# Optimization experiments

Hardware: AMD Instinct MI355X
Metric: run time of the kernel (lower is better)

Reference implementation:

```python
import jax, jax.numpy as jnp
import numpy as np

B, TQ, TKV, D, H = 4, 1024, 1024, 1024, 16
HD = D // H  # head_size = 64
EPS = 1e-5


def setup_inputs() -> dict:
    key = jax.random.key(0)
    ks = jax.random.split(key, 5)
    s = 0.02
    return {
        "x_q": jax.random.normal(ks[0], (B, TQ, D), jnp.float32),
        "x_kv": jax.random.normal(ks[1], (B, TKV, D), jnp.float32),
        "Wq": jax.random.normal(ks[2], (D, 2 * D), jnp.float32) * s,
        "Wkv": jax.random.normal(ks[3], (D, 3 * D), jnp.float32) * s,
        "Wc": jax.random.normal(ks[4], (D, D), jnp.float32) * s,
        "qn1": jnp.ones((HD,), jnp.float32),
        "kn1": jnp.ones((HD,), jnp.float32),
        "qn2": jnp.ones((HD,), jnp.float32),
        "kn2": jnp.ones((HD,), jnp.float32),
        "gn_w": jnp.ones((D,), jnp.float32),
        "gn_b": jnp.zeros((D,), jnp.float32),
        "lmb": jnp.full((1, H, 1, 1), -4.0, jnp.float32),
    }


def _rms(x, w):
    # RMSNorm over last dim (head_size), eps=1e-5, learned scale w
    return x * jax.lax.rsqrt(jnp.mean(x * x, axis=-1, keepdims=True) + EPS) * w


def _heads(t, T):
    # (B,T,D) -> (B,H,T,HD)
    return t.reshape(B, T, H, HD).transpose(0, 2, 1, 3)


def _attn(q, k, v):
    att = jnp.einsum('bhqd,bhkd->bhqk', q, k) * (1.0 / np.sqrt(HD))
    att = jax.nn.softmax(att, axis=-1)
    return jnp.einsum('bhqk,bhkd->bhqd', att, v)


def reference(x_q, x_kv, Wq, Wkv, Wc, qn1, kn1, qn2, kn2, gn_w, gn_b, lmb):
    q1, q2 = jnp.split(x_q @ Wq, 2, axis=-1)
    k1, k2, v = jnp.split(x_kv @ Wkv, 3, axis=-1)
    q1 = _rms(_heads(q1, TQ), qn1)
    q2 = _rms(_heads(q2, TQ), qn2)
    k1 = _rms(_heads(k1, TKV), kn1)
    k2 = _rms(_heads(k2, TKV), kn2)
    v = _heads(v, TKV)
    y = _attn(q1, k1, v) - jax.nn.softplus(lmb) * _attn(q2, k2, v)  # (B,H,TQ,HD)
    # GroupNorm(n_head groups over n_embd channels), input (B,C,TQ):
    # per (batch, head) stats over (TQ, HD)
    mu = jnp.mean(y, axis=(2, 3), keepdims=True)
    var = jnp.var(y, axis=(2, 3), keepdims=True)
    yn = (y - mu) * jax.lax.rsqrt(var + EPS)
    yn = yn * gn_w.reshape(1, H, 1, HD) + gn_b.reshape(1, H, 1, HD)
    y = yn.transpose(0, 2, 1, 3).reshape(B, TQ, D)
    return y @ Wc
```

## Files before the change

kernel.cpp:

```cpp
#include <hip/hip_runtime.h>
#include <cstdint>
#include <cstddef>

#define B_ 4
#define TQ_ 1024
#define TKV_ 1024
#define D_ 1024
#define H_ 16
#define HD_ 64

typedef __bf16 bf16_t;
typedef bf16_t bf16x4 __attribute__((ext_vector_type(4)));
typedef bf16_t bf16x8 __attribute__((ext_vector_type(8)));
typedef float f32x4 __attribute__((ext_vector_type(4)));

#if __has_builtin(__builtin_amdgcn_exp2f)
#define EXP2F __builtin_amdgcn_exp2f
#else
#define EXP2F exp2f
#endif

__device__ __forceinline__ bf16_t to_bf16(float f) {
  uint32_t u = __builtin_bit_cast(uint32_t, f);
  u += 0x7fffu + ((u >> 16) & 1u);
  uint16_t h = (uint16_t)(u >> 16);
  return __builtin_bit_cast(bf16_t, h);
}
__device__ __forceinline__ float bf2f(bf16_t b) {
  uint32_t u = ((uint32_t)__builtin_bit_cast(uint16_t, b)) << 16;
  return __builtin_bit_cast(float, u);
}
__device__ __forceinline__ uint32_t pack_bf16_trunc(float lo, float hi) {
  return __builtin_amdgcn_perm(__builtin_bit_cast(uint32_t, hi),
                               __builtin_bit_cast(uint32_t, lo), 0x07060302u);
}
__device__ __forceinline__ void gload_lds16(const void* g, void* l) {
  __builtin_amdgcn_global_load_lds((const __attribute__((address_space(1))) void*)g,
                                   (__attribute__((address_space(3))) void*)l, 16, 0, 0);
}

__global__ __launch_bounds__(256) void k_prep(const float* __restrict__ xq,
                                              const float* __restrict__ xkv,
                                              const float* __restrict__ Wq,
                                              const float* __restrict__ Wkv,
                                              const float* __restrict__ Wc,
                                              bf16_t* __restrict__ oq,
                                              bf16_t* __restrict__ okv,
                                              bf16_t* __restrict__ Wqt,
                                              bf16_t* __restrict__ Wkvt,
                                              bf16_t* __restrict__ Wct,
                                              float* __restrict__ part) {
  int blk = blockIdx.x;
  if (blk == 0 && threadIdx.x < 128) part[threadIdx.x] = 0.f;
  if (blk < 8192) {
    const float* in = (blk < 4096) ? xq : xkv;
    bf16_t* out = (blk < 4096) ? oq : okv;
    int i = (blk & 4095) * 256 + threadIdx.x;
    float4 v = ((const float4*)in)[i];
    bf16x4 o = {to_bf16(v.x), to_bf16(v.y), to_bf16(v.z), to_bf16(v.w)};
    *(bf16x4*)(out + (size_t)i * 4) = o;
  } else {
    __shared__ float tile[32][33];
    int t = blk - 8192;
    int x = t % 192, yb = t / 192;
    const float* in;
    bf16_t* out;
    int C, c0;
    if (x < 64) { in = Wq; out = Wqt; C = 2048; c0 = x * 32; }
    else if (x < 160) { in = Wkv; out = Wkvt; C = 3072; c0 = (x - 64) * 32; }
    else { in = Wc; out = Wct; C = 1024; c0 = (x - 160) * 32; }
    int r0 = yb * 32;
    int tx = threadIdx.x & 31, ty = threadIdx.x >> 5;
#pragma unroll
    for (int i = 0; i < 4; i++)
      tile[ty + i * 8][tx] = in[(size_t)(r0 + ty + i * 8) * C + c0 + tx];
    __syncthreads();
#pragma unroll
    for (int i = 0; i < 4; i++) {
      int rr = ty + i * 8;
      out[(size_t)(c0 + rr) * 1024 + r0 + tx] = to_bf16(tile[tx][rr]);
    }
  }
}

__global__ __launch_bounds__(256, 2) void k_gemm_qkv(const bf16_t* __restrict__ xq,
                                                     const bf16_t* __restrict__ xkv,
                                                     const bf16_t* __restrict__ Wqt,
                                                     const bf16_t* __restrict__ Wkvt,
                                                     const float* __restrict__ kn1,
                                                     const float* __restrict__ kn2,
                                                     bf16_t* __restrict__ q12,
                                                     bf16_t* __restrict__ k1h,
                                                     bf16_t* __restrict__ k2h,
                                                     bf16_t* __restrict__ vt) {
  __shared__ bf16_t As[128 * 32];
  __shared__ bf16_t Bs[128 * 32];
  const int tid = threadIdx.x;
  const int wave = tid >> 6, lane = tid & 63;
  const int ln = lane & 15, lq = lane >> 4;

  const int fid = blockIdx.x;
  const int xcd = fid & 7, l = fid >> 3;
  bool isq;
  int xb, yb;
  if (l < 64) {
    isq = true;
    xb = (xcd & 3) * 4 + (l & 3);
    yb = (xcd >> 2) * 16 + (l >> 2);
  } else {
    isq = false;
    int l2 = l - 64;
    xb = (xcd & 3) * 6 + l2 % 6;
    yb = (xcd >> 2) * 16 + l2 / 6;
  }
  const bf16_t* A = isq ? xq : xkv;
  const bf16_t* Bt = isq ? Wqt : Wkvt;
  const int n0 = xb * 128, m0 = yb * 128;
  const int wm = (wave >> 1) * 64, wn = (wave & 1) * 64;
  f32x4 acc[4][4];
#pragma unroll
  for (int i = 0; i < 4; i++)
#pragma unroll
    for (int j = 0; j < 4; j++) acc[i][j] = (f32x4){0.f, 0.f, 0.f, 0.f};

  for (int k0 = 0; k0 < 1024; k0 += 32) {
#pragma unroll
    for (int rnd = 0; rnd < 2; rnd++) {
      int c = rnd * 256 + tid;
      int row = c >> 2, col = (c & 3) * 8;
      int ldsoff = (rnd * 256 + wave * 64) * 16;
      gload_lds16(A + (size_t)(m0 + row) * 1024 + k0 + col, (char*)As + ldsoff);
      gload_lds16(Bt + (size_t)(n0 + row) * 1024 + k0 + col, (char*)Bs + ldsoff);
    }
    asm volatile("s_waitcnt vmcnt(0)" ::: "memory");
    __syncthreads();
    bf16x8 af[4], bfr[4];
#pragma unroll
    for (int i = 0; i < 4; i++) {
      af[i] = *(const bf16x8*)(As + (wm + i * 16 + ln) * 32 + lq * 8);
      bfr[i] = *(const bf16x8*)(Bs + (wn + i * 16 + ln) * 32 + lq * 8);
    }
#pragma unroll
    for (int i = 0; i < 4; i++)
#pragma unroll
      for (int j = 0; j < 4; j++)
        acc[i][j] = __builtin_amdgcn_mfma_f32_16x16x32_bf16(af[i], bfr[j], acc[i][j], 0, 0, 0);
    __syncthreads();
  }

  if (isq) {
#pragma unroll
    for (int i = 0; i < 4; i++)
#pragma unroll
      for (int j = 0; j < 4; j++)
#pragma unroll
        for (int r = 0; r < 4; r++) {
          int row = m0 + wm + i * 16 + lq * 4 + r;
          int col = n0 + wn + j * 16 + ln;
          q12[(size_t)row * 2048 + col] = to_bf16(acc[i][j][r]);
        }
  } else {
    const int col0 = n0 + wn;
    const int part3 = col0 >> 10;
    const int h = (col0 >> 6) & 15;
    const int b = m0 >> 10;
    const int bh = b * 16 + h;
    if (part3 < 2) {
      const float* kn = part3 ? kn2 : kn1;
      bf16_t* dst = part3 ? k2h : k1h;
      float kw[4];
#pragma unroll
      for (int j = 0; j < 4; j++) kw[j] = kn[j * 16 + ln];
#pragma unroll
      for (int i = 0; i < 4; i++)
#pragma unroll
        for (int r = 0; r < 4; r++) {
          float ss = 0.f;
#pragma unroll
          for (int j = 0; j < 4; j++) ss += acc[i][j][r] * acc[i][j][r];
          ss += __shfl_xor(ss, 1, 64);
          ss += __shfl_xor(ss, 2, 64);
          ss += __shfl_xor(ss, 4, 64);
          ss += __shfl_xor(ss, 8, 64);
          float rstd = rsqrtf(ss * (1.f / 64.f) + 1e-5f);
          int m = m0 + wm + i * 16 + lq * 4 + r;
          int t = m & 1023;
          size_t base = ((size_t)bh * 1024 + t) * 64;
#pragma unroll
          for (int j = 0; j < 4; j++)
            dst[base + j * 16 + ln] = to_bf16(acc[i][j][r] * rstd * kw[j]);
        }
    } else {
      bf16_t* obase = vt + (size_t)bh * 65536;
#pragma unroll
      for (int i = 0; i < 4; i++) {
        int t0 = (m0 & 1023) + wm + i * 16 + lq * 4;
        int tp = (t0 & ~31) | (((t0 >> 2) & 3) << 3) | (((t0 >> 4) & 1) << 2);
#pragma unroll
        for (int j = 0; j < 4; j++) {
          bf16x4 pv;
#pragma unroll
          for (int r = 0; r < 4; r++) pv[r] = to_bf16(acc[i][j][r]);
          *(bf16x4*)(obase + (size_t)(j * 16 + ln) * 1024 + tp) = pv;
        }
      }
    }
  }
}

__global__ __launch_bounds__(256, 2) void k_gemm64(const bf16_t* __restrict__ A,
                                                   const bf16_t* __restrict__ Bt,
                                                   float* __restrict__ C, int N, int K) {
  __shared__ bf16_t As[128 * 32];
  __shared__ bf16_t Bs[64 * 32];
  const int tid = threadIdx.x;
  const int wave = tid >> 6, lane = tid & 63;
  const int ln = lane & 15, lq = lane >> 4;
  const int fid = blockIdx.x;
  const int xcd = fid & 7, l = fid >> 3;
  const int lx = l & 1, ly = (l >> 1) & 15, yh = l >> 5;
  const int n0 = (xcd * 2 + lx) * 64;
  const int m0 = (yh * 16 + ly) * 128;
  const int wm = wave * 32;
  f32x4 acc[2][4];
#pragma unroll
  for (int i = 0; i < 2; i++)
#pragma unroll
    for (int j = 0; j < 4; j++) acc[i][j] = (f32x4){0.f, 0.f, 0.f, 0.f};

  for (int k0 = 0; k0 < K; k0 += 32) {
#pragma unroll
    for (int rnd = 0; rnd < 2; rnd++) {
      int c = rnd * 256 + tid;
      int row = c >> 2, col = (c & 3) * 8;
      int ldsoff = (rnd * 256 + wave * 64) * 16;
      gload_lds16(A + (size_t)(m0 + row) * K + k0 + col, (char*)As + ldsoff);
    }
    {
      int row = tid >> 2, col = (tid & 3) * 8;
      int ldsoff = (wave * 64) * 16;
      gload_lds16(Bt + (size_t)(n0 + row) * K + k0 + col, (char*)Bs + ldsoff);
    }
    asm volatile("s_waitcnt vmcnt(0)" ::: "memory");
    __syncthreads();
    bf16x8 af[2], bfr[4];
#pragma unroll
    for (int i = 0; i < 2; i++)
      af[i] = *(const bf16x8*)(As + (wm + i * 16 + ln) * 32 + lq * 8);
#pragma unroll
    for (int j = 0; j < 4; j++)
      bfr[j] = *(const bf16x8*)(Bs + (j * 16 + ln) * 32 + lq * 8);
#pragma unroll
    for (int i = 0; i < 2; i++)
#pragma unroll
      for (int j = 0; j < 4; j++)
        acc[i][j] = __builtin_amdgcn_mfma_f32_16x16x32_bf16(af[i], bfr[j], acc[i][j], 0, 0, 0);
    __syncthreads();
  }
#pragma unroll
  for (int i = 0; i < 2; i++)
#pragma unroll
    for (int j = 0; j < 4; j++)
#pragma unroll
      for (int r = 0; r < 4; r++) {
        int row = m0 + wm + i * 16 + lq * 4 + r;
        int col = n0 + j * 16 + ln;
        C[(size_t)row * N + col] = acc[i][j][r];
      }
}

__global__ __launch_bounds__(256, 2) void k_attn2(const bf16_t* __restrict__ q12,
                                                  const bf16_t* __restrict__ k1h,
                                                  const bf16_t* __restrict__ k2h,
                                                  const bf16_t* __restrict__ vt,
                                                  const float* __restrict__ qn1,
                                                  const float* __restrict__ qn2,
                                                  const float* __restrict__ lmb,
                                                  bf16_t* __restrict__ y,
                                                  float* __restrict__ part) {
  __shared__ bf16_t Ks[2][4096];
  __shared__ bf16_t Vs[4096];
  __shared__ float red[8];
  const int tid = threadIdx.x;
  const int wave = tid >> 6, lane = tid & 63;
  const int ln = lane & 15, lq = lane >> 4;
  const int swz = ln & 7;
  const int bh = blockIdx.x;
  const int b = bh >> 4, h = bh & 15;
  const int q0 = blockIdx.y * 128 + wave * 32;
  const bf16_t* kb[2] = {k1h + (size_t)bh * 65536, k2h + (size_t)bh * 65536};
  const bf16_t* vb = vt + (size_t)bh * 65536;

  bf16x8 qf[2][2][2];
#pragma unroll
  for (int st = 0; st < 2; st++)
#pragma unroll
    for (int mt = 0; mt < 2; mt++)
#pragma unroll
      for (int ks = 0; ks < 2; ks++)
        qf[st][mt][ks] = *(const bf16x8*)(q12 + (size_t)(b * 1024 + q0 + mt * 16 + ln) * 2048 +
                                          st * 1024 + h * 64 + ks * 32 + lq * 8);
#pragma unroll
  for (int st = 0; st < 2; st++)
#pragma unroll
    for (int mt = 0; mt < 2; mt++) {
      const float* qn = st ? qn2 : qn1;
      float ssq = 0.f;
#pragma unroll
      for (int ks = 0; ks < 2; ks++)
#pragma unroll
        for (int j = 0; j < 8; j++) {
          float v = bf2f(qf[st][mt][ks][j]);
          ssq += v * v;
        }
      ssq += __shfl_xor(ssq, 16, 64);
      ssq += __shfl_xor(ssq, 32, 64);
      float rr = rsqrtf(ssq * (1.f / 64.f) + 1e-5f) * (0.125f * 1.44269504f);
#pragma unroll
      for (int ks = 0; ks < 2; ks++)
#pragma unroll
        for (int j = 0; j < 8; j++)
          qf[st][mt][ks][j] = to_bf16(bf2f(qf[st][mt][ks][j]) * rr * qn[ks * 32 + lq * 8 + j]);
    }

  f32x4 O[2][2][4];
  float lp[2][2] = {{0.f, 0.f}, {0.f, 0.f}};
#pragma unroll
  for (int st = 0; st < 2; st++)
#pragma unroll
    for (int mt = 0; mt < 2; mt++)
#pragma unroll
      for (int nt = 0; nt < 4; nt++) O[st][mt][nt] = (f32x4){0.f, 0.f, 0.f, 0.f};

  for (int kv0 = 0; kv0 < TKV_; kv0 += 64) {
    __syncthreads();
#pragma unroll
    for (int r = 0; r < 6; r++) {
      int a = r >> 1, r2 = r & 1;
      int g = r2 * 256 + tid;
      int row = g >> 3;
      int blk = (g & 7) ^ (row & 7);
      const bf16_t* src = (a < 2) ? (kb[a] + (size_t)(kv0 + row) * 64 + blk * 8)
                                  : (vb + (size_t)row * 1024 + kv0 + blk * 8);
      char* dst = (a < 2) ? ((char*)Ks + a * 8192) : (char*)Vs;
      gload_lds16(src, dst + (r2 * 256 + wave * 64) * 16);
    }
    asm volatile("s_waitcnt vmcnt(0)" ::: "memory");
    __syncthreads();

    bf16x8 vf[2][4];
#pragma unroll
    for (int u = 0; u < 2; u++)
#pragma unroll
      for (int nt = 0; nt < 4; nt++)
        vf[u][nt] = *(const bf16x8*)(Vs + ((nt * 16 + ln) * 8 + ((u * 4 + lq) ^ swz)) * 8);

#pragma unroll
    for (int st = 0; st < 2; st++) {
      bf16x8 kf[2][4];
#pragma unroll
      for (int ks = 0; ks < 2; ks++)
#pragma unroll
        for (int t = 0; t < 4; t++)
          kf[ks][t] = *(const bf16x8*)(&Ks[st][((t * 16 + ln) * 8 + ((4 * ks + lq) ^ swz)) * 8]);
#pragma unroll
      for (int mt = 0; mt < 2; mt++) {
        f32x4 s[4];
#pragma unroll
        for (int t = 0; t < 4; t++) s[t] = (f32x4){0.f, 0.f, 0.f, 0.f};
#pragma unroll
        for (int ks = 0; ks < 2; ks++)
#pragma unroll
          for (int t = 0; t < 4; t++)
            s[t] = __builtin_amdgcn_mfma_f32_16x16x32_bf16(kf[ks][t], qf[st][mt][ks], s[t], 0, 0, 0);
        uint32_t pfu[2][4];
        float l = 0.f;
#pragma unroll
        for (int t = 0; t < 4; t++) {
          float e0 = EXP2F(s[t][0]), e1 = EXP2F(s[t][1]);
          float e2 = EXP2F(s[t][2]), e3 = EXP2F(s[t][3]);
          l += (e0 + e1) + (e2 + e3);
          pfu[t >> 1][(t & 1) * 2] = pack_bf16_trunc(e0, e1);
          pfu[t >> 1][(t & 1) * 2 + 1] = pack_bf16_trunc(e2, e3);
        }
        lp[st][mt] += l;
#pragma unroll
        for (int u = 0; u < 2; u++) {
          bf16x8 pf = __builtin_bit_cast(bf16x8, *(uint4*)pfu[u]);
#pragma unroll
          for (int nt = 0; nt < 4; nt++)
            O[st][mt][nt] =
                __builtin_amdgcn_mfma_f32_16x16x32_bf16(pf, vf[u][nt], O[st][mt][nt], 0, 0, 0);
        }
      }
    }
  }

  float c = log1pf(__expf(lmb[h]));
  float s_acc = 0.f, ss_acc = 0.f;
#pragma unroll
  for (int mt = 0; mt < 2; mt++) {
    float linv[2][4];
#pragma unroll
    for (int st = 0; st < 2; st++) {
      float l = lp[st][mt];
      l += __shfl_xor(l, 16, 64);
      l += __shfl_xor(l, 32, 64);
#pragma unroll
      for (int r = 0; r < 4; r++) linv[st][r] = 1.f / __shfl(l, lq * 4 + r, 64);
    }
#pragma unroll
    for (int nt = 0; nt < 4; nt++)
#pragma unroll
      for (int r = 0; r < 4; r++) {
        size_t a = ((size_t)bh * TQ_ + q0 + mt * 16 + lq * 4 + r) * 64 + nt * 16 + ln;
        float val = O[0][mt][nt][r] * linv[0][r] - c * O[1][mt][nt][r] * linv[1][r];
        s_acc += val;
        ss_acc += val * val;
        y[a] = to_bf16(val);
      }
  }
#pragma unroll
  for (int m = 1; m < 64; m <<= 1) {
    s_acc += __shfl_xor(s_acc, m, 64);
    ss_acc += __shfl_xor(ss_acc, m, 64);
  }
  if (lane == 0) {
    red[wave] = s_acc;
    red[4 + wave] = ss_acc;
  }
  __syncthreads();
  if (tid == 0) {
    atomicAdd(&part[bh * 2], red[0] + red[1] + red[2] + red[3]);
    atomicAdd(&part[bh * 2 + 1], red[4] + red[5] + red[6] + red[7]);
  }
}

__global__ __launch_bounds__(256) void k_gn_apply(const bf16_t* __restrict__ y,
                                                  const float* __restrict__ part,
                                                  const float* __restrict__ gw,
                                                  const float* __restrict__ gb,
                                                  bf16_t* __restrict__ yn) {
  int idx = blockIdx.x * 256 + threadIdx.x;
  int i = idx * 8;
  int bh = i >> 16;
  int h = bh & 15, b = bh >> 4;
  float S = part[bh * 2], SS = part[bh * 2 + 1];
  float mean = S * (1.f / 65536.f);
  float var = SS * (1.f / 65536.f) - mean * mean;
  float rstd = rsqrtf(var + 1e-5f);
  bf16x8 a = *(const bf16x8*)(y + i);
  int rem = i & 65535;
  int t = rem >> 6, d = rem & 63;
  bf16x8 o;
#pragma unroll
  for (int j = 0; j < 8; j++) {
    float f = (bf2f(a[j]) - mean) * rstd * gw[h * 64 + d + j] + gb[h * 64 + d + j];
    o[j] = to_bf16(f);
  }
  *(bf16x8*)(yn + ((size_t)(b * 1024 + t)) * 1024 + h * 64 + d) = o;
}

extern "C" void kernel_launch(void* const* d_in, const int* in_sizes, int n_in,
                              void* d_out, int out_size, void* d_ws, size_t ws_size,
                              hipStream_t stream) {
  const float* x_q = (const float*)d_in[0];
  const float* x_kv = (const float*)d_in[1];
  const float* Wq = (const float*)d_in[2];
  const float* Wkv = (const float*)d_in[3];
  const float* Wc = (const float*)d_in[4];
  const float* qn1 = (const float*)d_in[5];
  const float* kn1 = (const float*)d_in[6];
  const float* qn2 = (const float*)d_in[7];
  const float* kn2 = (const float*)d_in[8];
  const float* gn_w = (const float*)d_in[9];
  const float* gn_b = (const float*)d_in[10];
  const float* lmb = (const float*)d_in[11];

  const size_t MB = (size_t)1 << 20;
  char* ws = (char*)d_ws;
  bf16_t* xq_bf = (bf16_t*)(ws + 0 * MB);
  bf16_t* xkv_bf = (bf16_t*)(ws + 8 * MB);
  bf16_t* Wqt = (bf16_t*)(ws + 16 * MB);
  bf16_t* Wkvt = (bf16_t*)(ws + 20 * MB);
  bf16_t* Wct = (bf16_t*)(ws + 26 * MB);
  bf16_t* q12 = (bf16_t*)(ws + 28 * MB);
  bf16_t* k1h = (bf16_t*)(ws + 44 * MB);
  bf16_t* k2h = (bf16_t*)(ws + 52 * MB);
  bf16_t* vt = (bf16_t*)(ws + 60 * MB);
  bf16_t* y = (bf16_t*)(ws + 68 * MB);
  bf16_t* yn = (bf16_t*)(ws + 76 * MB);
  float* part = (float*)(ws + 84 * MB);

  k_prep<<<14336, 256, 0, stream>>>(x_q, x_kv, Wq, Wkv, Wc, xq_bf, xkv_bf, Wqt, Wkvt, Wct,
                                    part);
  k_gemm_qkv<<<1280, 256, 0, stream>>>(xq_bf, xkv_bf, Wqt, Wkvt, kn1, kn2, q12, k1h, k2h,
                                       vt);
  k_attn2<<<dim3(64, 8), 256, 0, stream>>>(q12, k1h, k2h, vt, qn1, qn2, lmb, y, part);
  k_gn_apply<<<2048, 256, 0, stream>>>(y, part, gn_w, gn_b, yn);
  k_gemm64<<<512, 256, 0, stream>>>(yn, Wct, (float*)d_out, 1024, 1024);
}
```

Before: 238.3 us.

## Double K-step depth in GEMMs and attention, add XOR-swizzled LDS layout

The QKV and output GEMMs now stage 64-wide K slices per iteration instead of 32. Their LDS tiles use an XOR swizzle on 16-byte chunks to avoid bank conflicts. The attention kernel loads 128 KV rows per iteration instead of 64 and processes them in two inner chunks. The aim is to halve the number of barrier/wait round trips and add LDS bank-conflict avoidance in the GEMMs. The cost is doubled shared memory per block, which could lower occupancy below the two blocks per CU the launch bounds target.

```diff
diff --git a/kernel.cpp b/kernel.cpp
--- a/kernel.cpp
+++ b/kernel.cpp
@@ -93,11 +93,12 @@
                                                      bf16_t* __restrict__ k1h,
                                                      bf16_t* __restrict__ k2h,
                                                      bf16_t* __restrict__ vt) {
-  __shared__ bf16_t As[128 * 32];
-  __shared__ bf16_t Bs[128 * 32];
+  __shared__ bf16_t As[128 * 64];
+  __shared__ bf16_t Bs[128 * 64];
   const int tid = threadIdx.x;
   const int wave = tid >> 6, lane = tid & 63;
   const int ln = lane & 15, lq = lane >> 4;
+  const int swz = ln & 7;
 
   const int fid = blockIdx.x;
   const int xcd = fid & 7, l = fid >> 3;
@@ -123,28 +124,33 @@
 #pragma unroll
     for (int j = 0; j < 4; j++) acc[i][j] = (f32x4){0.f, 0.f, 0.f, 0.f};
 
-  for (int k0 = 0; k0 < 1024; k0 += 32) {
-#pragma unroll
-    for (int rnd = 0; rnd < 2; rnd++) {
-      int c = rnd * 256 + tid;
-      int row = c >> 2, col = (c & 3) * 8;
-      int ldsoff = (rnd * 256 + wave * 64) * 16;
-      gload_lds16(A + (size_t)(m0 + row) * 1024 + k0 + col, (char*)As + ldsoff);
-      gload_lds16(Bt + (size_t)(n0 + row) * 1024 + k0 + col, (char*)Bs + ldsoff);
+  for (int k0 = 0; k0 < 1024; k0 += 64) {
+#pragma unroll
+    for (int r = 0; r < 8; r++) {
+      int g = (r & 3) * 256 + tid;
+      int row = g >> 3;
+      int dg = (g & 7) ^ (row & 7);
+      const bf16_t* src = (r < 4) ? (A + (size_t)(m0 + row) * 1024 + k0 + dg * 8)
+                                  : (Bt + (size_t)(n0 + row) * 1024 + k0 + dg * 8);
+      char* dst = ((r < 4) ? (char*)As : (char*)Bs) + ((r & 3) * 256 + wave * 64) * 16;
+      gload_lds16(src, dst);
     }
     asm volatile("s_waitcnt vmcnt(0)" ::: "memory");
     __syncthreads();
-    bf16x8 af[4], bfr[4];
-#pragma unroll
-    for (int i = 0; i < 4; i++) {
-      af[i] = *(const bf16x8*)(As + (wm + i * 16 + ln) * 32 + lq * 8);
-      bfr[i] = *(const bf16x8*)(Bs + (wn + i * 16 + ln) * 32 + lq * 8);
-    }
-#pragma unroll
-    for (int i = 0; i < 4; i++)
-#pragma unroll
-      for (int j = 0; j < 4; j++)
-        acc[i][j] = __builtin_amdgcn_mfma_f32_16x16x32_bf16(af[i], bfr[j], acc[i][j], 0, 0, 0);
+#pragma unroll
+    for (int ks = 0; ks < 2; ks++) {
+      bf16x8 af[4], bfr[4];
+#pragma unroll
+      for (int i = 0; i < 4; i++) {
+        af[i] = *(const bf16x8*)(As + ((wm + i * 16 + ln) * 8 + ((ks * 4 + lq) ^ swz)) * 8);
+        bfr[i] = *(const bf16x8*)(Bs + ((wn + i * 16 + ln) * 8 + ((ks * 4 + lq) ^ swz)) * 8);
+      }
+#pragma unroll
+      for (int i = 0; i < 4; i++)
+#pragma unroll
+        for (int j = 0; j < 4; j++)
+          acc[i][j] = __builtin_amdgcn_mfma_f32_16x16x32_bf16(af[i], bfr[j], acc[i][j], 0, 0, 0);
+    }
     __syncthreads();
   }
 
@@ -211,11 +217,12 @@
 __global__ __launch_bounds__(256, 2) void k_gemm64(const bf16_t* __restrict__ A,
                                                    const bf16_t* __restrict__ Bt,
                                                    float* __restrict__ C, int N, int K) {
-  __shared__ bf16_t As[128 * 32];
-  __shared__ bf16_t Bs[64 * 32];
+  __shared__ bf16_t As[128 * 64];
+  __shared__ bf16_t Bs[64 * 64];
   const int tid = threadIdx.x;
   const int wave = tid >> 6, lane = tid & 63;
   const int ln = lane & 15, lq = lane >> 4;
+  const int swz = ln & 7;
   const int fid = blockIdx.x;
   const int xcd = fid & 7, l = fid >> 3;
   const int lx = l & 1, ly = (l >> 1) & 15, yh = l >> 5;
@@ -228,33 +235,35 @@
 #pragma unroll
     for (int j = 0; j < 4; j++) acc[i][j] = (f32x4){0.f, 0.f, 0.f, 0.f};
 
-  for (int k0 = 0; k0 < K; k0 += 32) {
-#pragma unroll
-    for (int rnd = 0; rnd < 2; rnd++) {
-      int c = rnd * 256 + tid;
-      int row = c >> 2, col = (c & 3) * 8;
-      int ldsoff = (rnd * 256 + wave * 64) * 16;
-      gload_lds16(A + (size_t)(m0 + row) * K + k0 + col, (char*)As + ldsoff);
-    }
-    {
-      int row = tid >> 2, col = (tid & 3) * 8;
-      int ldsoff = (wave * 64) * 16;
-      gload_lds16(Bt + (size_t)(n0 + row) * K + k0 + col, (char*)Bs + ldsoff);
+  for (int k0 = 0; k0 < K; k0 += 64) {
+#pragma unroll
+    for (int r = 0; r < 6; r++) {
+      int g = ((r < 4) ? (r & 3) : (r - 4)) * 256 + tid;
+      int row = g >> 3;
+      int dg = (g & 7) ^ (row & 7);
+      const bf16_t* src = (r < 4) ? (A + (size_t)(m0 + row) * K + k0 + dg * 8)
+                                  : (Bt + (size_t)(n0 + row) * K + k0 + dg * 8);
+      char* dst = ((r < 4) ? (char*)As + (r & 3) * 4096 : (char*)Bs + (r - 4) * 4096) +
+                  (wave * 64) * 16;
+      gload_lds16(src, dst);
     }
     asm volatile("s_waitcnt vmcnt(0)" ::: "memory");
     __syncthreads();
-    bf16x8 af[2], bfr[4];
-#pragma unroll
-    for (int i = 0; i < 2; i++)
-      af[i] = *(const bf16x8*)(As + (wm + i * 16 + ln) * 32 + lq * 8);
-#pragma unroll
-    for (int j = 0; j < 4; j++)
-      bfr[j] = *(const bf16x8*)(Bs + (j * 16 + ln) * 32 + lq * 8);
-#pragma unroll
-    for (int i = 0; i < 2; i++)
+#pragma unroll
+    for (int ks = 0; ks < 2; ks++) {
+      bf16x8 af[2], bfr[4];
+#pragma unroll
+      for (int i = 0; i < 2; i++)
+        af[i] = *(const bf16x8*)(As + ((wm + i * 16 + ln) * 8 + ((ks * 4 + lq) ^ swz)) * 8);
 #pragma unroll
       for (int j = 0; j < 4; j++)
-        acc[i][j] = __builtin_amdgcn_mfma_f32_16x16x32_bf16(af[i], bfr[j], acc[i][j], 0, 0, 0);
+        bfr[j] = *(const bf16x8*)(Bs + ((j * 16 + ln) * 8 + ((ks * 4 + lq) ^ swz)) * 8);
+#pragma unroll
+      for (int i = 0; i < 2; i++)
+#pragma unroll
+        for (int j = 0; j < 4; j++)
+          acc[i][j] = __builtin_amdgcn_mfma_f32_16x16x32_bf16(af[i], bfr[j], acc[i][j], 0, 0, 0);
+    }
     __syncthreads();
   }
 #pragma unroll
@@ -278,8 +287,8 @@
                                                   const float* __restrict__ lmb,
                                                   bf16_t* __restrict__ y,
                                                   float* __restrict__ part) {
-  __shared__ bf16_t Ks[2][4096];
-  __shared__ bf16_t Vs[4096];
+  __shared__ bf16_t Ks[2][8192];
+  __shared__ bf16_t Vs[8192];
   __shared__ float red[8];
   const int tid = threadIdx.x;
   const int wave = tid >> 6, lane = tid & 63;
@@ -332,65 +341,78 @@
 #pragma unroll
       for (int nt = 0; nt < 4; nt++) O[st][mt][nt] = (f32x4){0.f, 0.f, 0.f, 0.f};
 
-  for (int kv0 = 0; kv0 < TKV_; kv0 += 64) {
-    __syncthreads();
-#pragma unroll
-    for (int r = 0; r < 6; r++) {
-      int a = r >> 1, r2 = r & 1;
-      int g = r2 * 256 + tid;
-      int row = g >> 3;
-      int blk = (g & 7) ^ (row & 7);
-      const bf16_t* src = (a < 2) ? (kb[a] + (size_t)(kv0 + row) * 64 + blk * 8)
-                                  : (vb + (size_t)row * 1024 + kv0 + blk * 8);
-      char* dst = (a < 2) ? ((char*)Ks + a * 8192) : (char*)Vs;
-      gload_lds16(src, dst + (r2 * 256 + wave * 64) * 16);
+  for (int kv0 = 0; kv0 < TKV_; kv0 += 128) {
+    __syncthreads();
+#pragma unroll
+    for (int r = 0; r < 12; r++) {
+      int reg = r >> 2;
+      int g = (r & 3) * 256 + tid;
+      const bf16_t* src;
+      if (reg < 2) {
+        int row = g >> 3;
+        int dg = (g & 7) ^ (row & 7);
+        src = kb[reg] + (size_t)(kv0 + row) * 64 + dg * 8;
+      } else {
+        int row = g >> 4;
+        int p = g & 15;
+        int dg = (p & 8) | ((p & 7) ^ (row & 7));
+        src = vb + (size_t)row * 1024 + kv0 + dg * 8;
+      }
+      char* dst = ((reg < 2) ? (char*)Ks[reg] : (char*)Vs) + ((r & 3) * 256 + wave * 64) * 16;
+      gload_lds16(src, dst);
     }
     asm volatile("s_waitcnt vmcnt(0)" ::: "memory");
     __syncthreads();
 
-    bf16x8 vf[2][4];
-#pragma unroll
-    for (int u = 0; u < 2; u++)
-#pragma unroll
-      for (int nt = 0; nt < 4; nt++)
-        vf[u][nt] = *(const bf16x8*)(Vs + ((nt * 16 + ln) * 8 + ((u * 4 + lq) ^ swz)) * 8);
-
-#pragma unroll
-    for (int st = 0; st < 2; st++) {
-      bf16x8 kf[2][4];
-#pragma unroll
-      for (int ks = 0; ks < 2; ks++)
-#pragma unroll
-        for (int t = 0; t < 4; t++)
-          kf[ks][t] = *(const bf16x8*)(&Ks[st][((t * 16 + ln) * 8 + ((4 * ks + lq) ^ swz)) * 8]);
-#pragma unroll
-      for (int mt = 0; mt < 2; mt++) {
-        f32x4 s[4];
-#pragma unroll
-        for (int t = 0; t < 4; t++) s[t] = (f32x4){0.f, 0.f, 0.f, 0.f};
+#pragma unroll
+    for (int cc = 0; cc < 2; cc++) {
+      bf16x8 vf[2][4];
+#pragma unroll
+      for (int u = 0; u < 2; u++)
+#pragma unroll
+        for (int nt = 0; nt < 4; nt++)
+          vf[u][nt] =
+              *(const bf16x8*)(Vs + ((nt * 16 + ln) * 16 + cc * 8 + ((u * 4 + lq) ^ swz)) * 8);
+
+#pragma unroll
+      for (int st = 0; st < 2; st++) {
+        bf16x8 kf[2][4];
 #pragma unroll
         for (int ks = 0; ks < 2; ks++)
 #pragma unroll
           for (int t = 0; t < 4; t++)
-            s[t] = __builtin_amdgcn_mfma_f32_16x16x32_bf16(kf[ks][t], qf[st][mt][ks], s[t], 0, 0, 0);
-        uint32_t pfu[2][4];
-        float l = 0.f;
-#pragma unroll
-        for (int t = 0; t < 4; t++) {
-          float e0 = EXP2F(s[t][0]), e1 = EXP2F(s[t][1]);
-          float e2 = EXP2F(s[t][2]), e3 = EXP2F(s[t][3]);
-          l += (e0 + e1) + (e2 + e3);
-          pfu[t >> 1][(t & 1) * 2] = pack_bf16_trunc(e0, e1);
-          pfu[t >> 1][(t & 1) * 2 + 1] = pack_bf16_trunc(e2, e3);
-        }
-        lp[st][mt] += l;
-#pragma unroll
-        for (int u = 0; u < 2; u++) {
-          bf16x8 pf = __builtin_bit_cast(bf16x8, *(uint4*)pfu[u]);
-#pragma unroll
-          for (int nt = 0; nt < 4; nt++)
-            O[st][mt][nt] =
-                __builtin_amdgcn_mfma_f32_16x16x32_bf16(pf, vf[u][nt], O[st][mt][nt], 0, 0, 0);
+            kf[ks][t] = *(const bf16x8*)(&Ks[st][((cc * 64 + t * 16 + ln) * 8 +
+                                                  ((ks * 4 + lq) ^ swz)) * 8]);
+#pragma unroll
+        for (int mt = 0; mt < 2; mt++) {
+          f32x4 s[4];
+#pragma unroll
+          for (int t = 0; t < 4; t++) s[t] = (f32x4){0.f, 0.f, 0.f, 0.f};
+#pragma unroll
+          for (int ks = 0; ks < 2; ks++)
+#pragma unroll
+            for (int t = 0; t < 4; t++)
+              s[t] =
+                  __builtin_amdgcn_mfma_f32_16x16x32_bf16(kf[ks][t], qf[st][mt][ks], s[t], 0, 0, 0);
+          uint32_t pfu[2][4];
+          float l = 0.f;
+#pragma unroll
+          for (int t = 0; t < 4; t++) {
+            float e0 = EXP2F(s[t][0]), e1 = EXP2F(s[t][1]);
+            float e2 = EXP2F(s[t][2]), e3 = EXP2F(s[t][3]);
+            l += (e0 + e1) + (e2 + e3);
+            pfu[t >> 1][(t & 1) * 2] = pack_bf16_trunc(e0, e1);
+            pfu[t >> 1][(t & 1) * 2 + 1] = pack_bf16_trunc(e2, e3);
+          }
+          lp[st][mt] += l;
+#pragma unroll
+          for (int u = 0; u < 2; u++) {
+            bf16x8 pf = __builtin_bit_cast(bf16x8, *(uint4*)pfu[u]);
+#pragma unroll
+            for (int nt = 0; nt < 4; nt++)
+              O[st][mt][nt] =
+                  __builtin_amdgcn_mfma_f32_16x16x32_bf16(pf, vf[u][nt], O[st][mt][nt], 0, 0, 0);
+          }
         }
       }
     }
```

Result: slower. 279.8 us (+17.4%).
